# Optimization experiments

Hardware: AMD Instinct MI355X
Metric: run time of the kernel (lower is better)

Reference implementation:

```python
import jax, jax.numpy as jnp
import numpy as np

D_MODEL = 1024
NUM_HEADS = 16
D_K = D_MODEL // NUM_HEADS
THETA = 10000.0
SEQ = 2048
BATCH = 2


def _rope(t, positions):
    # t: [b, h, s, d_k]; positions: [s]
    half = D_K // 2
    freqs = 1.0 / (THETA ** (jnp.arange(0, D_K, 2, dtype=jnp.float32) / D_K))  # [half]
    angles = positions.astype(jnp.float32)[:, None] * freqs[None, :]  # [s, half]
    cos = jnp.cos(angles)  # [s, half]
    sin = jnp.sin(angles)
    tr = t.reshape(t.shape[:-1] + (half, 2))  # pairs are (even, odd) interleaved
    x1, x2 = tr[..., 0], tr[..., 1]
    r1 = x1 * cos - x2 * sin
    r2 = x1 * sin + x2 * cos
    return jnp.stack([r1, r2], axis=-1).reshape(t.shape)


def setup_inputs() -> dict:
    key = jax.random.key(0)
    ks = jax.random.split(key, 5)
    std = float(np.sqrt(2.0 / (D_MODEL + D_MODEL)))
    return {
        "x": jax.random.normal(ks[0], (BATCH, SEQ, D_MODEL), dtype=jnp.float32),
        "token_positions": jnp.arange(SEQ, dtype=jnp.int64 if jax.config.jax_enable_x64 else jnp.int32),
        "wq": std * jax.random.normal(ks[1], (D_MODEL, D_MODEL), dtype=jnp.float32),
        "wk": std * jax.random.normal(ks[2], (D_MODEL, D_MODEL), dtype=jnp.float32),
        "wv": std * jax.random.normal(ks[3], (D_MODEL, D_MODEL), dtype=jnp.float32),
        "wo": std * jax.random.normal(ks[4], (D_MODEL, D_MODEL), dtype=jnp.float32),
    }


def reference(x, token_positions, wq, wk, wv, wo):
    b, s, _ = x.shape
    # projections: weight is (d_out, d_in), y = x @ W^T
    def proj(w):
        y = jnp.einsum('bsd,od->bso', x, w)
        return y.reshape(b, s, NUM_HEADS, D_K).transpose(0, 2, 1, 3)  # [b,h,s,dk]
    Q, K, V = proj(wq), proj(wk), proj(wv)
    Q = _rope(Q, token_positions)
    K = _rope(K, token_positions)
    scale = 1.0 / jnp.sqrt(jnp.asarray(D_K, dtype=x.dtype))
    scores = jnp.einsum('bhqd,bhkd->bhqk', Q, K) * scale  # [b,h,s,s]
    causal = jnp.tril(jnp.ones((s, s), dtype=bool))
    scores = jnp.where(causal, scores, jnp.asarray(-jnp.inf, dtype=scores.dtype))
    attn = jax.nn.softmax(scores, axis=-1)
    out = jnp.einsum('bhqk,bhkd->bhqd', attn, V)  # [b,h,s,dk]
    out = out.transpose(0, 2, 1, 3).reshape(b, s, D_MODEL)
    return jnp.einsum('bsd,od->bso', out, wo)
```

## Files before the change

kernel.cpp:

```cpp
#include <hip/hip_runtime.h>
#include <hip/hip_bf16.h>
#include <math.h>

#define BATCH  2
#define SEQ    2048
#define DMODEL 1024
#define NHEADS 16
#define DK     64

typedef __hip_bfloat16 bf16;
typedef short s16x8 __attribute__((ext_vector_type(8)));
typedef float f32x4 __attribute__((ext_vector_type(4)));

union P8 { int4 i4; s16x8 v; short s[8]; };

static __device__ __forceinline__ unsigned short f2bu(float f) {
    bf16 h = __float2bfloat16(f);
    return *reinterpret_cast<unsigned short*>(&h);
}

static __device__ __forceinline__ void gll16(const void* g, void* l) {
    __builtin_amdgcn_global_load_lds(
        (const __attribute__((address_space(1))) unsigned int*)g,
        (__attribute__((address_space(3))) unsigned int*)l, 16, 0, 0);
}

__global__ __launch_bounds__(256) void conv_k(
    const float* __restrict__ x, const float* __restrict__ wq,
    const float* __restrict__ wk, const float* __restrict__ wv,
    const float* __restrict__ wo, bf16* __restrict__ dst)
{
    const size_t e0 = ((size_t)blockIdx.x * 256 + threadIdx.x) << 3;
    const float* src;
    bf16* d;
    if (e0 < (size_t)4194304) { src = x + e0; d = dst + e0; }
    else {
        const size_t r = e0 - 4194304;
        const int wsel = (int)(r >> 20);
        const size_t off = r & 1048575;
        src = (wsel == 0 ? wq : wsel == 1 ? wk : wsel == 2 ? wv : wo) + off;
        d = dst + 4194304 + ((size_t)wsel << 20) + off;
    }
    const float4 a = *(const float4*)src;
    const float4 b = *(const float4*)(src + 4);
    P8 p;
    p.s[0] = (short)f2bu(a.x); p.s[1] = (short)f2bu(a.y);
    p.s[2] = (short)f2bu(a.z); p.s[3] = (short)f2bu(a.w);
    p.s[4] = (short)f2bu(b.x); p.s[5] = (short)f2bu(b.y);
    p.s[6] = (short)f2bu(b.z); p.s[7] = (short)f2bu(b.w);
    *(int4*)d = p.i4;
}

__global__ __launch_bounds__(256) void gemm_qkv(
    const bf16* __restrict__ Ab, const bf16* __restrict__ Wb,
    bf16* __restrict__ O0, bf16* __restrict__ O1, bf16* __restrict__ O2)
{
    __shared__ __align__(16) short As[128 * 64];
    __shared__ __align__(16) short Ws[128 * 64];
    const int tid  = threadIdx.x;
    const int w    = tid >> 6;
    const int lane = tid & 63;
    const int ln   = lane & 15;
    const int quad = lane >> 4;
    const int id   = blockIdx.x;
    const int m_base = (id & 31) << 7;
    const int n_base = ((id >> 5) & 7) << 7;
    const int z = id >> 8;
    const bf16* Wz = Wb + ((size_t)z << 20);

    const int lrw = lane >> 3;
    const int lcs = ((lane & 7) ^ lrw) << 3;
    const size_t abase = (size_t)(m_base + 32 * w + lrw) * DMODEL + lcs;
    const size_t wbase = (size_t)(n_base + 32 * w + lrw) * DMODEL + lcs;
    short* ldsA = &As[2048 * w];
    short* ldsW = &Ws[2048 * w];

    const f32x4 zero4 = {0.f, 0.f, 0.f, 0.f};
    f32x4 acc[4][4];
    #pragma unroll
    for (int i = 0; i < 4; ++i)
        #pragma unroll
        for (int j = 0; j < 4; ++j) acc[i][j] = zero4;

    const int mo = (w >> 1) << 6, no = (w & 1) << 6;
    const int swz = ln & 7;

    for (int k0 = 0; k0 < DMODEL; k0 += 64) {
        __syncthreads();
        #pragma unroll
        for (int t = 0; t < 4; ++t) {
            gll16(Ab + abase + (size_t)t * 8 * DMODEL + k0, ldsA + t * 512);
            gll16(Wz + wbase + (size_t)t * 8 * DMODEL + k0, ldsW + t * 512);
        }
        __syncthreads();
        #pragma unroll
        for (int t = 0; t < 2; ++t) {
            const int co = (((t << 2) + quad) ^ swz) << 3;
            s16x8 af[4], bw[4];
            #pragma unroll
            for (int i = 0; i < 4; ++i) {
                af[i] = *(const s16x8*)&As[(mo + 16 * i + ln) * 64 + co];
                bw[i] = *(const s16x8*)&Ws[(no + 16 * i + ln) * 64 + co];
            }
            #pragma unroll
            for (int mi = 0; mi < 4; ++mi)
                #pragma unroll
                for (int ni = 0; ni < 4; ++ni)
                    acc[mi][ni] = __builtin_amdgcn_mfma_f32_16x16x32_bf16(
                        af[mi], bw[ni], acc[mi][ni], 0, 0, 0);
        }
    }

    if (z < 2) {
        bf16* C = (z == 0) ? O0 : O1;
        const float qs = (z == 0) ? 0.125f : 1.0f;
        const int h = (n_base + no) >> 6;
        const float sgn = (ln & 1) ? 1.0f : -1.0f;
        float freq[4];
        #pragma unroll
        for (int ni = 0; ni < 4; ++ni)
            freq[ni] = exp2f(-(float)((16 * ni + ln) >> 1) * 0.4152410119f);
        #pragma unroll
        for (int mi = 0; mi < 4; ++mi) {
            #pragma unroll
            for (int r = 0; r < 4; ++r) {
                const int m = m_base + mo + 16 * mi + quad * 4 + r;
                const int b = m >> 11, s = m & (SEQ - 1);
                const float fs = (float)s;
                float sn[4], cs[4];
                #pragma unroll
                for (int ni = 0; ni < 4; ++ni)
                    __sincosf(fs * freq[ni], &sn[ni], &cs[ni]);
                bf16* row = C + (((size_t)(b * NHEADS + h) * SEQ) + s) * DK;
                #pragma unroll
                for (int ni = 0; ni < 4; ++ni) {
                    const float v = acc[mi][ni][r];
                    const float p = __shfl_xor(v, 1, 64);
                    row[16 * ni + ln] =
                        __float2bfloat16((v * cs[ni] + sgn * p * sn[ni]) * qs);
                }
            }
        }
    } else {
        #pragma unroll
        for (int ni = 0; ni < 4; ++ni) {
            const int n = n_base + no + 16 * ni + ln;
            const int h = n >> 6, d = n & (DK - 1);
            #pragma unroll
            for (int mi = 0; mi < 4; ++mi) {
                const int m0v = m_base + mo + 16 * mi + quad * 4;
                const int b = m0v >> 11, s0 = m0v & (SEQ - 1);
                ushort4 pk;
                pk.x = f2bu(acc[mi][ni][0]); pk.y = f2bu(acc[mi][ni][1]);
                pk.z = f2bu(acc[mi][ni][2]); pk.w = f2bu(acc[mi][ni][3]);
                *(ushort4*)(O2 + (((size_t)(b * NHEADS + h) * DK) + d) * SEQ + s0) = pk;
            }
        }
    }
}

__global__ __launch_bounds__(256) void gemm_wo(
    const bf16* __restrict__ Ab, const bf16* __restrict__ Wb,
    float* __restrict__ Of)
{
    __shared__ __align__(16) short As[64 * 64];
    __shared__ __align__(16) short Ws[128 * 64];
    const int tid  = threadIdx.x;
    const int w    = tid >> 6;
    const int lane = tid & 63;
    const int ln   = lane & 15;
    const int quad = lane >> 4;
    const int id   = blockIdx.x;
    const int m_base = (id & 63) << 6;
    const int n_base = (id >> 6) << 7;

    const int lrw = lane >> 3;
    const int lcs = ((lane & 7) ^ lrw) << 3;
    const int am = m_base + 16 * w + lrw;
    short* ldsA = &As[1024 * w];
    const size_t wbase = (size_t)(n_base + 32 * w + lrw) * DMODEL + lcs;
    short* ldsW = &Ws[2048 * w];

    const f32x4 zero4 = {0.f, 0.f, 0.f, 0.f};
    f32x4 acc[2][4];
    #pragma unroll
    for (int i = 0; i < 2; ++i)
        #pragma unroll
        for (int j = 0; j < 4; ++j) acc[i][j] = zero4;

    const int mo = (w >> 1) << 5, no = (w & 1) << 6;
    const int swz = ln & 7;

    for (int k0 = 0; k0 < DMODEL; k0 += 64) {
        const int hh = k0 >> 6;
        __syncthreads();
        #pragma unroll
        for (int t = 0; t < 2; ++t) {
            const int m = am + t * 8;
            const int b = m >> 11, s = m & (SEQ - 1);
            gll16(Ab + (((size_t)(b * NHEADS + hh) * SEQ) + s) * DK + lcs,
                  ldsA + t * 512);
        }
        #pragma unroll
        for (int t = 0; t < 4; ++t)
            gll16(Wb + wbase + (size_t)t * 8 * DMODEL + k0, ldsW + t * 512);
        __syncthreads();
        #pragma unroll
        for (int t = 0; t < 2; ++t) {
            const int co = (((t << 2) + quad) ^ swz) << 3;
            s16x8 af[2], bw[4];
            #pragma unroll
            for (int i = 0; i < 2; ++i)
                af[i] = *(const s16x8*)&As[(mo + 16 * i + ln) * 64 + co];
            #pragma unroll
            for (int j = 0; j < 4; ++j)
                bw[j] = *(const s16x8*)&Ws[(no + 16 * j + ln) * 64 + co];
            #pragma unroll
            for (int mi = 0; mi < 2; ++mi)
                #pragma unroll
                for (int ni = 0; ni < 4; ++ni)
                    acc[mi][ni] = __builtin_amdgcn_mfma_f32_16x16x32_bf16(
                        af[mi], bw[ni], acc[mi][ni], 0, 0, 0);
        }
    }

    #pragma unroll
    for (int mi = 0; mi < 2; ++mi)
        #pragma unroll
        for (int ni = 0; ni < 4; ++ni) {
            const int n = n_base + no + 16 * ni + ln;
            #pragma unroll
            for (int r = 0; r < 4; ++r) {
                const int m = m_base + mo + 16 * mi + quad * 4 + r;
                Of[(size_t)m * DMODEL + n] = acc[mi][ni][r];
            }
        }
}

__global__ __launch_bounds__(256) void attn_k(bf16* __restrict__ Q,
                                              const bf16* __restrict__ Kg,
                                              const bf16* __restrict__ VT)
{
    __shared__ __align__(16) short Ks[64 * 72];
    __shared__ __align__(16) short Vs[64 * 72];
    __shared__ __align__(16) short PT[64 * 72];
    const int tid  = threadIdx.x;
    const int w    = tid >> 6;
    const int lane = tid & 63;
    const int ln   = lane & 15;
    const int quad = lane >> 4;
    const int bh = blockIdx.x & 31;
    const int qt = 31 - (blockIdx.x >> 5);
    const size_t base = (size_t)bh * (SEQ * DK);
    const int srow = tid >> 2;
    const int sc   = (tid & 3) << 4;
    const int qrow = qt * 64 + 16 * w + ln;

    P8 qa0, qa1;
    {
        const bf16* qsrc = Q + base + (size_t)qrow * DK + quad * 8;
        qa0.i4 = *(const int4*)(qsrc);
        qa1.i4 = *(const int4*)(qsrc + 32);
    }
    const f32x4 zero4 = {0.f, 0.f, 0.f, 0.f};
    f32x4 o[4];
    #pragma unroll
    for (int mt = 0; mt < 4; ++mt) o[mt] = zero4;
    float lsum = 0.f;

    P8 kk[2], vv[2];
    {
        const bf16* ksrc = Kg + base + (size_t)srow * DK + sc;
        kk[0].i4 = *(const int4*)(ksrc);
        kk[1].i4 = *(const int4*)(ksrc + 8);
        const bf16* vsrc = VT + base + (size_t)srow * SEQ + sc;
        vv[0].i4 = *(const int4*)(vsrc);
        vv[1].i4 = *(const int4*)(vsrc + 8);
    }

    for (int kb = 0; kb <= qt; ++kb) {
        __syncthreads();
        *(s16x8*)&Ks[srow * 72 + sc]     = kk[0].v;
        *(s16x8*)&Ks[srow * 72 + sc + 8] = kk[1].v;
        *(s16x8*)&Vs[srow * 72 + sc]     = vv[0].v;
        *(s16x8*)&Vs[srow * 72 + sc + 8] = vv[1].v;
        __syncthreads();

        if (kb < qt) {
            const bf16* ksrc = Kg + base + (size_t)((kb + 1) * 64 + srow) * DK + sc;
            kk[0].i4 = *(const int4*)(ksrc);
            kk[1].i4 = *(const int4*)(ksrc + 8);
            const bf16* vsrc = VT + base + (size_t)srow * SEQ + (kb + 1) * 64 + sc;
            vv[0].i4 = *(const int4*)(vsrc);
            vv[1].i4 = *(const int4*)(vsrc + 8);
        }

        f32x4 sf[4];
        #pragma unroll
        for (int mt = 0; mt < 4; ++mt) {
            sf[mt] = zero4;
            s16x8 ka  = *(const s16x8*)&Ks[(16 * mt + ln) * 72 + quad * 8];
            s16x8 kb2 = *(const s16x8*)&Ks[(16 * mt + ln) * 72 + 32 + quad * 8];
            sf[mt] = __builtin_amdgcn_mfma_f32_16x16x32_bf16(ka,  qa0.v, sf[mt], 0, 0, 0);
            sf[mt] = __builtin_amdgcn_mfma_f32_16x16x32_bf16(kb2, qa1.v, sf[mt], 0, 0, 0);
        }

        if (kb == qt) {
            #pragma unroll
            for (int mt = 0; mt < 4; ++mt)
                #pragma unroll
                for (int r = 0; r < 4; ++r)
                    if (kb * 64 + 16 * mt + quad * 4 + r > qrow) sf[mt][r] = -INFINITY;
        }
        #pragma unroll
        for (int mt = 0; mt < 4; ++mt)
            #pragma unroll
            for (int r = 0; r < 4; ++r) {
                sf[mt][r] = __expf(sf[mt][r]);
                lsum += sf[mt][r];
            }

        #pragma unroll
        for (int mt = 0; mt < 4; ++mt) {
            ushort4 pk;
            pk.x = f2bu(sf[mt][0]); pk.y = f2bu(sf[mt][1]);
            pk.z = f2bu(sf[mt][2]); pk.w = f2bu(sf[mt][3]);
            *(ushort4*)&PT[(16 * w + ln) * 72 + 16 * mt + quad * 4] = pk;
        }

        s16x8 pa0 = *(const s16x8*)&PT[(16 * w + ln) * 72 + quad * 8];
        s16x8 pa1 = *(const s16x8*)&PT[(16 * w + ln) * 72 + 32 + quad * 8];
        #pragma unroll
        for (int mt = 0; mt < 4; ++mt) {
            s16x8 va0 = *(const s16x8*)&Vs[(16 * mt + ln) * 72 + quad * 8];
            s16x8 va1 = *(const s16x8*)&Vs[(16 * mt + ln) * 72 + 32 + quad * 8];
            o[mt] = __builtin_amdgcn_mfma_f32_16x16x32_bf16(va0, pa0, o[mt], 0, 0, 0);
            o[mt] = __builtin_amdgcn_mfma_f32_16x16x32_bf16(va1, pa1, o[mt], 0, 0, 0);
        }
    }

    lsum += __shfl_xor(lsum, 16, 64);
    lsum += __shfl_xor(lsum, 32, 64);
    const float inv = 1.0f / lsum;
    #pragma unroll
    for (int mt = 0; mt < 4; ++mt) {
        ushort4 st;
        st.x = f2bu(o[mt][0] * inv); st.y = f2bu(o[mt][1] * inv);
        st.z = f2bu(o[mt][2] * inv); st.w = f2bu(o[mt][3] * inv);
        *(ushort4*)(Q + base + (size_t)qrow * DK + 16 * mt + quad * 4) = st;
    }
}

extern "C" void kernel_launch(void* const* d_in, const int* in_sizes, int n_in,
                              void* d_out, int out_size, void* d_ws, size_t ws_size,
                              hipStream_t stream)
{
    const float* x  = (const float*)d_in[0];
    const float* wq = (const float*)d_in[2];
    const float* wk = (const float*)d_in[3];
    const float* wv = (const float*)d_in[4];
    const float* wo = (const float*)d_in[5];

    bf16* wsb   = (bf16*)d_ws;
    bf16* xb    = wsb;
    bf16* wqkvb = wsb + ((size_t)4 << 20);
    bf16* wob   = wsb + ((size_t)7 << 20);
    bf16* Qw    = wsb + ((size_t)8 << 20);
    bf16* Kw    = wsb + ((size_t)12 << 20);
    bf16* VTw   = wsb + ((size_t)16 << 20);

    conv_k<<<4096, 256, 0, stream>>>(x, wq, wk, wv, wo, wsb);
    gemm_qkv<<<768, 256, 0, stream>>>(xb, wqkvb, Qw, Kw, VTw);
    attn_k<<<1024, 256, 0, stream>>>(Qw, Kw, VTw);
    gemm_wo<<<512, 256, 0, stream>>>(Qw, wob, (float*)d_out);
}
```

Measured before the change: 174.7 us.

## Rewrite QKV GEMM as 256x256 double-buffered ping-pong pipeline with XCD-aware remap

Replaces the 128x128, 4-wave QKV projection GEMM with a 256x256-tile, 8-wave kernel. The K tiles are double-buffered in LDS, and quarter-tile global→LDS loads are interleaved with MFMA phases under explicit barriers, vmcnt/lgkmcnt waits and s_setprio. Block IDs are remapped so neighbouring tiles land on the same XCD, aiming for better L2 reuse. The goal is to hide load latency and raise arithmetic intensity per block. In exchange the grid drops to 192 blocks, fewer than the CU count, and each block needs 128KB of LDS, so occupancy and load balance may suffer.

```diff
diff --git a/kernel.cpp b/kernel.cpp
--- a/kernel.cpp
+++ b/kernel.cpp
@@ -24,6 +24,12 @@
         (const __attribute__((address_space(1))) unsigned int*)g,
         (__attribute__((address_space(3))) unsigned int*)l, 16, 0, 0);
 }
+
+#define BAR()    __builtin_amdgcn_s_barrier()
+#define LGKM0()  do { asm volatile("s_waitcnt lgkmcnt(0)" ::: "memory"); \
+                      __builtin_amdgcn_sched_barrier(0); } while (0)
+#define WVM(n)   do { asm volatile("s_waitcnt vmcnt(" #n ")" ::: "memory"); \
+                      __builtin_amdgcn_sched_barrier(0); } while (0)
 
 __global__ __launch_bounds__(256) void conv_k(
     const float* __restrict__ x, const float* __restrict__ wq,
@@ -51,108 +57,183 @@
     *(int4*)d = p.i4;
 }
 
-__global__ __launch_bounds__(256) void gemm_qkv(
+__global__ __launch_bounds__(512, 2) void gemm_qkv(
     const bf16* __restrict__ Ab, const bf16* __restrict__ Wb,
     bf16* __restrict__ O0, bf16* __restrict__ O1, bf16* __restrict__ O2)
 {
-    __shared__ __align__(16) short As[128 * 64];
-    __shared__ __align__(16) short Ws[128 * 64];
+    __shared__ __align__(16) short As[2][256 * 64];
+    __shared__ __align__(16) short Ws[2][256 * 64];
     const int tid  = threadIdx.x;
-    const int w    = tid >> 6;
+    const int wid  = tid >> 6;
     const int lane = tid & 63;
     const int ln   = lane & 15;
     const int quad = lane >> 4;
-    const int id   = blockIdx.x;
-    const int m_base = (id & 31) << 7;
-    const int n_base = ((id >> 5) & 7) << 7;
-    const int z = id >> 8;
+    const int wr   = wid >> 2;
+    const int wc   = wid & 3;
+    const int swz  = ln & 7;
+
+    const int orig = blockIdx.x;
+    const int wg = (orig & 7) * 24 + (orig >> 3);
+    const int m_base = (wg & 15) << 8;
+    const int nz = wg >> 4;
+    const int z  = nz >> 2;
+    const int n_base = (nz & 3) << 8;
     const bf16* Wz = Wb + ((size_t)z << 20);
 
     const int lrw = lane >> 3;
     const int lcs = ((lane & 7) ^ lrw) << 3;
-    const size_t abase = (size_t)(m_base + 32 * w + lrw) * DMODEL + lcs;
-    const size_t wbase = (size_t)(n_base + 32 * w + lrw) * DMODEL + lcs;
-    short* ldsA = &As[2048 * w];
-    short* ldsW = &Ws[2048 * w];
+
+    auto stageHalf = [&](int b, int kt, int q) {
+        if (kt >= 16) return;
+        const int rs = (q & 1) * 128 + wid * 16;
+        if (q < 2) {
+            const size_t src = (size_t)(m_base + rs + lrw) * DMODEL
+                             + (size_t)(kt * 64 + lcs);
+            short* d = &As[b][rs * 64];
+            gll16(Ab + src,              d);
+            gll16(Ab + src + 8 * DMODEL, d + 8 * 64);
+        } else {
+            const size_t src = (size_t)(n_base + rs + lrw) * DMODEL
+                             + (size_t)(kt * 64 + lcs);
+            short* d = &Ws[b][rs * 64];
+            gll16(Wz + src,              d);
+            gll16(Wz + src + 8 * DMODEL, d + 8 * 64);
+        }
+    };
 
     const f32x4 zero4 = {0.f, 0.f, 0.f, 0.f};
-    f32x4 acc[4][4];
+    f32x4 acc[8][4];
     #pragma unroll
-    for (int i = 0; i < 4; ++i)
+    for (int i = 0; i < 8; ++i)
         #pragma unroll
         for (int j = 0; j < 4; ++j) acc[i][j] = zero4;
 
-    const int mo = (w >> 1) << 6, no = (w & 1) << 6;
-    const int swz = ln & 7;
-
-    for (int k0 = 0; k0 < DMODEL; k0 += 64) {
-        __syncthreads();
-        #pragma unroll
-        for (int t = 0; t < 4; ++t) {
-            gll16(Ab + abase + (size_t)t * 8 * DMODEL + k0, ldsA + t * 512);
-            gll16(Wz + wbase + (size_t)t * 8 * DMODEL + k0, ldsW + t * 512);
-        }
-        __syncthreads();
-        #pragma unroll
-        for (int t = 0; t < 2; ++t) {
-            const int co = (((t << 2) + quad) ^ swz) << 3;
-            s16x8 af[4], bw[4];
-            #pragma unroll
-            for (int i = 0; i < 4; ++i) {
-                af[i] = *(const s16x8*)&As[(mo + 16 * i + ln) * 64 + co];
-                bw[i] = *(const s16x8*)&Ws[(no + 16 * i + ln) * 64 + co];
-            }
-            #pragma unroll
-            for (int mi = 0; mi < 4; ++mi)
+    s16x8 af[4][2], bw01[2][2], bw23[2][2];
+
+    auto readA = [&](const short* Sb, int mg) {
+        #pragma unroll
+        for (int mi = 0; mi < 4; ++mi)
+            #pragma unroll
+            for (int kk = 0; kk < 2; ++kk)
+                af[mi][kk] = *(const s16x8*)&Sb[
+                    (wr * 128 + mg * 64 + 16 * mi + ln) * 64 +
+                    ((((kk << 2) + quad) ^ swz) << 3)];
+    };
+    auto readB = [&](const short* Sb, int np, s16x8 (&bwp)[2][2]) {
+        #pragma unroll
+        for (int nj = 0; nj < 2; ++nj)
+            #pragma unroll
+            for (int kk = 0; kk < 2; ++kk)
+                bwp[nj][kk] = *(const s16x8*)&Sb[
+                    (wc * 64 + np * 32 + 16 * nj + ln) * 64 +
+                    ((((kk << 2) + quad) ^ swz) << 3)];
+    };
+    auto mmac = [&](int mg, int np, const s16x8 (&bwp)[2][2]) {
+        #pragma unroll
+        for (int mi = 0; mi < 4; ++mi)
+            #pragma unroll
+            for (int nj = 0; nj < 2; ++nj)
                 #pragma unroll
-                for (int ni = 0; ni < 4; ++ni)
-                    acc[mi][ni] = __builtin_amdgcn_mfma_f32_16x16x32_bf16(
-                        af[mi], bw[ni], acc[mi][ni], 0, 0, 0);
-        }
+                for (int kk = 0; kk < 2; ++kk)
+                    acc[mg * 4 + mi][np * 2 + nj] =
+                        __builtin_amdgcn_mfma_f32_16x16x32_bf16(
+                            af[mi][kk], bwp[nj][kk],
+                            acc[mg * 4 + mi][np * 2 + nj], 0, 0, 0);
+    };
+
+    stageHalf(0, 0, 0); stageHalf(0, 0, 1);
+    stageHalf(0, 0, 2); stageHalf(0, 0, 3);
+    stageHalf(1, 1, 0);
+    WVM(2);
+    BAR();
+
+    #pragma unroll 1
+    for (int i = 0; i < 8; ++i) {
+        const int ta = 2 * i, tb = 2 * i + 1;
+        readA(As[0], 0); readB(Ws[0], 0, bw01);
+        stageHalf(1, tb, 1);
+        BAR(); LGKM0();
+        __builtin_amdgcn_s_setprio(1); mmac(0, 0, bw01);
+        __builtin_amdgcn_s_setprio(0); BAR();
+        readB(Ws[0], 1, bw23);
+        stageHalf(1, tb, 2);
+        BAR(); LGKM0();
+        __builtin_amdgcn_s_setprio(1); mmac(0, 1, bw23);
+        __builtin_amdgcn_s_setprio(0); BAR();
+        readA(As[0], 1);
+        stageHalf(1, tb, 3);
+        BAR(); LGKM0();
+        __builtin_amdgcn_s_setprio(1); mmac(1, 0, bw01);
+        __builtin_amdgcn_s_setprio(0); BAR();
+        stageHalf(0, ta + 2, 0);
+        if (i < 7) { WVM(2); } else { WVM(0); }
+        BAR();
+        __builtin_amdgcn_s_setprio(1); mmac(1, 1, bw23);
+        __builtin_amdgcn_s_setprio(0); BAR();
+        readA(As[1], 0); readB(Ws[1], 0, bw01);
+        stageHalf(0, ta + 2, 1);
+        BAR(); LGKM0();
+        __builtin_amdgcn_s_setprio(1); mmac(0, 0, bw01);
+        __builtin_amdgcn_s_setprio(0); BAR();
+        readB(Ws[1], 1, bw23);
+        stageHalf(0, ta + 2, 2);
+        BAR(); LGKM0();
+        __builtin_amdgcn_s_setprio(1); mmac(0, 1, bw23);
+        __builtin_amdgcn_s_setprio(0); BAR();
+        readA(As[1], 1);
+        stageHalf(0, ta + 2, 3);
+        BAR(); LGKM0();
+        __builtin_amdgcn_s_setprio(1); mmac(1, 0, bw01);
+        __builtin_amdgcn_s_setprio(0); BAR();
+        stageHalf(1, tb + 2, 0);
+        if (i < 7) { WVM(2); } else { WVM(0); }
+        BAR();
+        __builtin_amdgcn_s_setprio(1); mmac(1, 1, bw23);
+        __builtin_amdgcn_s_setprio(0); BAR();
     }
 
     if (z < 2) {
         bf16* C = (z == 0) ? O0 : O1;
         const float qs = (z == 0) ? 0.125f : 1.0f;
-        const int h = (n_base + no) >> 6;
+        const int h = (n_base >> 6) + wc;
         const float sgn = (ln & 1) ? 1.0f : -1.0f;
         float freq[4];
         #pragma unroll
-        for (int ni = 0; ni < 4; ++ni)
-            freq[ni] = exp2f(-(float)((16 * ni + ln) >> 1) * 0.4152410119f);
-        #pragma unroll
-        for (int mi = 0; mi < 4; ++mi) {
+        for (int nj = 0; nj < 4; ++nj)
+            freq[nj] = exp2f(-(float)((16 * nj + ln) >> 1) * 0.4152410119f);
+        #pragma unroll
+        for (int mi = 0; mi < 8; ++mi) {
             #pragma unroll
             for (int r = 0; r < 4; ++r) {
-                const int m = m_base + mo + 16 * mi + quad * 4 + r;
+                const int m = m_base + wr * 128 + 16 * mi + quad * 4 + r;
                 const int b = m >> 11, s = m & (SEQ - 1);
                 const float fs = (float)s;
                 float sn[4], cs[4];
                 #pragma unroll
-                for (int ni = 0; ni < 4; ++ni)
-                    __sincosf(fs * freq[ni], &sn[ni], &cs[ni]);
+                for (int nj = 0; nj < 4; ++nj)
+                    __sincosf(fs * freq[nj], &sn[nj], &cs[nj]);
                 bf16* row = C + (((size_t)(b * NHEADS + h) * SEQ) + s) * DK;
                 #pragma unroll
-                for (int ni = 0; ni < 4; ++ni) {
-                    const float v = acc[mi][ni][r];
+                for (int nj = 0; nj < 4; ++nj) {
+                    const float v = acc[mi][nj][r];
                     const float p = __shfl_xor(v, 1, 64);
-                    row[16 * ni + ln] =
-                        __float2bfloat16((v * cs[ni] + sgn * p * sn[ni]) * qs);
+                    row[16 * nj + ln] =
+                        __float2bfloat16((v * cs[nj] + sgn * p * sn[nj]) * qs);
                 }
             }
         }
     } else {
         #pragma unroll
-        for (int ni = 0; ni < 4; ++ni) {
-            const int n = n_base + no + 16 * ni + ln;
+        for (int nj = 0; nj < 4; ++nj) {
+            const int n = n_base + wc * 64 + 16 * nj + ln;
             const int h = n >> 6, d = n & (DK - 1);
             #pragma unroll
-            for (int mi = 0; mi < 4; ++mi) {
-                const int m0v = m_base + mo + 16 * mi + quad * 4;
+            for (int mi = 0; mi < 8; ++mi) {
+                const int m0v = m_base + wr * 128 + 16 * mi + quad * 4;
                 const int b = m0v >> 11, s0 = m0v & (SEQ - 1);
                 ushort4 pk;
-                pk.x = f2bu(acc[mi][ni][0]); pk.y = f2bu(acc[mi][ni][1]);
-                pk.z = f2bu(acc[mi][ni][2]); pk.w = f2bu(acc[mi][ni][3]);
+                pk.x = f2bu(acc[mi][nj][0]); pk.y = f2bu(acc[mi][nj][1]);
+                pk.z = f2bu(acc[mi][nj][2]); pk.w = f2bu(acc[mi][nj][3]);
                 *(ushort4*)(O2 + (((size_t)(b * NHEADS + h) * DK) + d) * SEQ + s0) = pk;
             }
         }
@@ -164,7 +245,7 @@
     float* __restrict__ Of)
 {
     __shared__ __align__(16) short As[64 * 64];
-    __shared__ __align__(16) short Ws[128 * 64];
+    __shared__ __align__(16) short Ws2[128 * 64];
     const int tid  = threadIdx.x;
     const int w    = tid >> 6;
     const int lane = tid & 63;
@@ -179,7 +260,7 @@
     const int am = m_base + 16 * w + lrw;
     short* ldsA = &As[1024 * w];
     const size_t wbase = (size_t)(n_base + 32 * w + lrw) * DMODEL + lcs;
-    short* ldsW = &Ws[2048 * w];
+    short* ldsW = &Ws2[2048 * w];
 
     const f32x4 zero4 = {0.f, 0.f, 0.f, 0.f};
     f32x4 acc[2][4];
@@ -214,7 +295,7 @@
                 af[i] = *(const s16x8*)&As[(mo + 16 * i + ln) * 64 + co];
             #pragma unroll
             for (int j = 0; j < 4; ++j)
-                bw[j] = *(const s16x8*)&Ws[(no + 16 * j + ln) * 64 + co];
+                bw[j] = *(const s16x8*)&Ws2[(no + 16 * j + ln) * 64 + co];
             #pragma unroll
             for (int mi = 0; mi < 2; ++mi)
                 #pragma unroll
@@ -370,7 +451,7 @@
     bf16* VTw   = wsb + ((size_t)16 << 20);
 
     conv_k<<<4096, 256, 0, stream>>>(x, wq, wk, wv, wo, wsb);
-    gemm_qkv<<<768, 256, 0, stream>>>(xb, wqkvb, Qw, Kw, VTw);
+    gemm_qkv<<<192, 512, 0, stream>>>(xb, wqkvb, Qw, Kw, VTw);
     attn_k<<<1024, 256, 0, stream>>>(Qw, Kw, VTw);
     gemm_wo<<<512, 256, 0, stream>>>(Qw, wob, (float*)d_out);
 }
```

After: 175.9 us. No clear change (+0.7%).
